# Kernel optimization log

Measured on AMD Instinct MI355X. Metric: run time of the kernel, lower is better.

## Reference

```python
import jax, jax.numpy as jnp
import numpy as np

B, S, D = 8, 2048, 512
DK, DV = 64, 64

def setup_inputs() -> dict:
    key = jax.random.key(0)
    ks = jax.random.split(key, 9)
    glorot = lambda k, shape: jax.random.uniform(k, shape, jnp.float32, -1.0, 1.0) * np.sqrt(6.0 / (shape[0] + shape[-1] if len(shape) > 1 else shape[0] + 1))
    return {
        "x_q": jax.random.normal(ks[0], (B, S, D), jnp.float32),
        "x_k": jax.random.normal(ks[1], (B, S, D), jnp.float32),
        "x_v": jax.random.normal(ks[2], (B, S, D), jnp.float32),
        "Wq": glorot(ks[3], (D, DK)), "bq": glorot(ks[4], (DK,)),
        "Wk": glorot(ks[5], (D, DK)), "bk": glorot(ks[6], (DK,)),
        "Wv": glorot(ks[7], (D, DV)), "bv": glorot(ks[8], (DV,)),
    }

def reference(x_q, x_k, x_v, Wq, bq, Wk, bk, Wv, bv):
    q = jnp.einsum("bsd,dk->bsk", x_q, Wq) + bq          # [B,S,DK]
    k = jnp.einsum("bsd,dk->bsk", x_k, Wk) + bk          # [B,S,DK]
    v = jnp.einsum("bsd,dv->bsv", x_v, Wv) + bv          # [B,S,DV]
    scale = 1.0 / np.sqrt(DK).astype(np.float32)
    scores = jnp.einsum("bqk,bsk->bqs", q, k) * scale     # [B,S,S]
    attn = jax.nn.softmax(scores, axis=-1)
    return jnp.einsum("bqs,bsv->bqv", attn, v)            # [B,S,DV]
```

## Files before the change

### kernel.cpp

```cpp
#include <hip/hip_runtime.h>
#include <stdint.h>

typedef __bf16 bf16;
typedef __bf16 bf16x8 __attribute__((ext_vector_type(8)));
typedef float f32x4 __attribute__((ext_vector_type(4)));

struct alignas(8) U16x4 { uint16_t v[4]; };

__device__ __forceinline__ f32x4 mfma16(bf16x8 a, bf16x8 b, f32x4 c) {
    return __builtin_amdgcn_mfma_f32_16x16x32_bf16(a, b, c, 0, 0, 0);
}

__device__ __forceinline__ void gload_lds16(const void* g, void* l) {
    __builtin_amdgcn_global_load_lds(
        (const __attribute__((address_space(1))) uint32_t*)g,
        (__attribute__((address_space(3))) uint32_t*)l, 16, 0, 0);
}

__device__ __forceinline__ uint16_t bf_bits(bf16 v) {
    return __builtin_bit_cast(uint16_t, v);
}

__device__ __forceinline__ float bf2f(uint16_t u) {
    uint32_t x = (uint32_t)u << 16;
    return __builtin_bit_cast(float, x);
}

#define QSCALE 0.18033688011112042f

__global__ __launch_bounds__(256, 2)
void proj_kernel(const float* __restrict__ xq, const float* __restrict__ xk,
                 const float* __restrict__ xv,
                 const float* __restrict__ Wq, const float* __restrict__ bq,
                 const float* __restrict__ Wk, const float* __restrict__ bk,
                 const float* __restrict__ Wv, const float* __restrict__ bv,
                 uint16_t* __restrict__ q_ws, uint16_t* __restrict__ k_ws,
                 uint16_t* __restrict__ vt_ws)
{
    const int p = blockIdx.y;
    const float* x    = (p == 0) ? xq : (p == 1) ? xk : xv;
    const float* W    = (p == 0) ? Wq : (p == 1) ? Wk : Wv;
    const float* bias = (p == 0) ? bq : (p == 1) ? bk : bv;

    const int m0 = blockIdx.x * 64;
    const int t  = threadIdx.x;
    const int l  = t & 63;
    const int w  = t >> 6;

    __shared__ __align__(16) uint16_t sW[32768];

    const int arow = m0 + w * 16 + (l & 15);
    const int kg   = (l >> 4) * 8;
    const float* xrow = x + (size_t)arow * 512 + kg;

    float4 av0[8], av1[8];
    #pragma unroll
    for (int s = 0; s < 8; s++) {
        av0[s] = *(const float4*)(xrow + s * 32);
        av1[s] = *(const float4*)(xrow + s * 32 + 4);
    }

    {
        const int f2 = (t >> 6) & 3;
        const int n  = (t & 15) + 16 * f2;
        const int kq = ((t >> 4) & 3) * 8;
        #pragma unroll 4
        for (int r = 0; r < 16; r++) {
            const int k0 = r * 32 + kq;
            bf16x8 v;
            #pragma unroll
            for (int j = 0; j < 8; j++)
                v[j] = (bf16)W[(size_t)(k0 + j) * 64 + n];
            *(bf16x8*)((char*)sW + (r * 256 + t) * 16) = v;
        }
    }

    __syncthreads();

    f32x4 acc[4];
    const f32x4 zero = {0.f, 0.f, 0.f, 0.f};
    #pragma unroll
    for (int f = 0; f < 4; f++) acc[f] = zero;

    #pragma unroll
    for (int kt = 0; kt < 16; kt++) {
        const int slot = kt & 7;
        bf16x8 a;
        a[0] = (bf16)av0[slot].x; a[1] = (bf16)av0[slot].y;
        a[2] = (bf16)av0[slot].z; a[3] = (bf16)av0[slot].w;
        a[4] = (bf16)av1[slot].x; a[5] = (bf16)av1[slot].y;
        a[6] = (bf16)av1[slot].z; a[7] = (bf16)av1[slot].w;
        if (kt < 8) {
            const int kb = (kt + 8) * 32;
            av0[slot] = *(const float4*)(xrow + kb);
            av1[slot] = *(const float4*)(xrow + kb + 4);
        }
        #pragma unroll
        for (int f = 0; f < 4; f++) {
            bf16x8 bfr = *(const bf16x8*)((const char*)sW + ((kt * 4 + f) * 64 + l) * 16);
            acc[f] = mfma16(a, bfr, acc[f]);
        }
    }

    float bv4[4];
    #pragma unroll
    for (int f = 0; f < 4; f++) bv4[f] = bias[16 * f + (l & 15)];

    if (p < 2) {
        uint16_t* outp = (p == 0) ? q_ws : k_ws;
        const float scale = (p == 0) ? QSCALE : 1.0f;
        #pragma unroll
        for (int f = 0; f < 4; f++)
            #pragma unroll
            for (int r = 0; r < 4; r++) {
                const int row = m0 + w * 16 + (l >> 4) * 4 + r;
                const int col = 16 * f + (l & 15);
                outp[(size_t)row * 64 + col] = bf_bits((bf16)((acc[f][r] + bv4[f]) * scale));
            }
    } else {
        #pragma unroll
        for (int f = 0; f < 4; f++) {
            const int row0 = m0 + w * 16 + (l >> 4) * 4;
            const int col  = 16 * f + (l & 15);
            const int bb = row0 >> 11;
            const int s0 = row0 & 2047;
            U16x4 pk;
            #pragma unroll
            for (int r = 0; r < 4; r++)
                pk.v[r] = bf_bits((bf16)(acc[f][r] + bv4[f]));
            *(U16x4*)(vt_ws + ((size_t)bb * 64 + col) * 2048 + s0) = pk;
        }
    }
}

template <int NCHUNK>
__global__ __launch_bounds__(512, 4)
void attn_kernel(const uint16_t* __restrict__ q_ws, const uint16_t* __restrict__ k_ws,
                 const uint16_t* __restrict__ vt_ws, float* __restrict__ out,
                 uint16_t* __restrict__ O_part, float* __restrict__ l_arr)
{
    constexpr int NT = 32 / NCHUNK;
    const int qt = blockIdx.x, b = blockIdx.y, c = blockIdx.z;
    const int t = threadIdx.x, l = t & 63, w = t >> 6;
    const int q = l & 15, g = l >> 4;
    const int q0 = qt * 128;

    __shared__ __align__(16) uint16_t sK[2][64 * 64];
    __shared__ __align__(16) uint16_t sV[2][64 * 64];
    __shared__ __align__(16) uint16_t sP[8][16 * 72];

    const uint16_t* qp = q_ws + ((size_t)(b * 2048 + q0)) * 64;
    const uint16_t* kp = k_ws + (size_t)b * 2048 * 64;
    const uint16_t* vp = vt_ws + (size_t)b * 64 * 2048;

    bf16x8 aq[2];
    #pragma unroll
    for (int ks = 0; ks < 2; ks++)
        aq[ks] = *(const bf16x8*)(qp + (size_t)(w * 16 + q) * 64 + g * 8 + ks * 32);

    const f32x4 zero = {0.f, 0.f, 0.f, 0.f};
    f32x4 acco[4];
    #pragma unroll
    for (int f = 0; f < 4; f++) acco[f] = zero;
    float l_st = 0.f;

    auto stage = [&](int tile, int buf) {
        const int kv0  = tile * 64;
        const int row  = t >> 3;
        const int slot = (t & 7) ^ (row & 7);
        gload_lds16(kp + (size_t)(kv0 + row) * 64 + slot * 8,
                    (char*)sK[buf] + t * 16);
        gload_lds16(vp + (size_t)row * 2048 + kv0 + slot * 8,
                    (char*)sV[buf] + t * 16);
    };

    stage(c * NT, 0);
    __syncthreads();

    for (int i = 0; i < NT; i++) {
        const int buf = i & 1;
        if (i < NT - 1) stage(c * NT + i + 1, buf ^ 1);

        f32x4 accs[4];
        #pragma unroll
        for (int f = 0; f < 4; f++) accs[f] = zero;
        #pragma unroll
        for (int ks = 0; ks < 2; ks++) {
            const int kb = g * 16 + ks * 64;
            #pragma unroll
            for (int f = 0; f < 4; f++) {
                const int srow = q + 16 * f;
                bf16x8 bk = *(const bf16x8*)((const char*)sK[buf] + srow * 128 + (kb ^ ((srow & 7) << 4)));
                accs[f] = mfma16(bk, aq[ks], accs[f]);
            }
        }

        float rs = 0.f;
        #pragma unroll
        for (int f = 0; f < 4; f++) {
            U16x4 pk;
            #pragma unroll
            for (int r = 0; r < 4; r++) {
                const float pv = exp2f(accs[f][r]);
                rs += pv;
                pk.v[r] = bf_bits((bf16)pv);
            }
            const int byte = q * 144 + ((32 * f + 8 * g) ^ ((q & 7) << 4));
            *(U16x4*)((char*)sP[w] + byte) = pk;
        }
        rs += __shfl_xor(rs, 16);
        rs += __shfl_xor(rs, 32);
        l_st += rs;

        asm volatile("s_waitcnt lgkmcnt(0)" ::: "memory");

        #pragma unroll
        for (int ks = 0; ks < 2; ks++) {
            bf16x8 ap = *(const bf16x8*)((const char*)sP[w] + q * 144 + ((ks * 64 + g * 16) ^ ((q & 7) << 4)));
            const int kb = g * 16 + ks * 64;
            #pragma unroll
            for (int f = 0; f < 4; f++) {
                const int vrow = q + 16 * f;
                bf16x8 bv2 = *(const bf16x8*)((const char*)sV[buf] + vrow * 128 + (kb ^ ((vrow & 7) << 4)));
                acco[f] = mfma16(ap, bv2, acco[f]);
            }
        }
        __syncthreads();
    }

    if constexpr (NCHUNK == 1) {
        #pragma unroll
        for (int r = 0; r < 4; r++) {
            const float lb = __shfl(l_st, (g * 4 + r) + (l & 48));
            #pragma unroll
            for (int f = 0; f < 4; f++) {
                const int qrow = q0 + w * 16 + g * 4 + r;
                const int col  = 16 * f + q;
                out[((size_t)(b * 2048 + qrow)) * 64 + col] = acco[f][r] / lb;
            }
        }
    } else {
        #pragma unroll
        for (int f = 0; f < 4; f++)
            #pragma unroll
            for (int r = 0; r < 4; r++) {
                const int qrow = q0 + w * 16 + g * 4 + r;
                const int col  = 16 * f + q;
                O_part[((size_t)c * 16384 + b * 2048 + qrow) * 64 + col] =
                    bf_bits((bf16)acco[f][r]);
            }
        if (l < 16) {
            const size_t idx = (size_t)c * 16384 + b * 2048 + q0 + w * 16 + l;
            l_arr[idx] = l_st;
        }
    }
}

__global__ __launch_bounds__(256, 8)
void combine_kernel(const uint16_t* __restrict__ O_part,
                    const float* __restrict__ l_arr, float* __restrict__ out)
{
    const int b = blockIdx.y;
    const int r0 = (blockIdx.x >> 2) * 64 + (blockIdx.x & 3) * 16;
    const int t = threadIdx.x;
    const int col = t & 63;
    const int rg = t >> 6;

    #pragma unroll
    for (int pass = 0; pass < 4; pass++) {
        const int qrow = r0 + pass * 4 + rg;
        const size_t ridx = (size_t)b * 2048 + qrow;
        float L = 0.f;
        #pragma unroll
        for (int c = 0; c < 4; c++) L += l_arr[(size_t)c * 16384 + ridx];
        float acc = 0.f;
        #pragma unroll
        for (int c = 0; c < 4; c++)
            acc += bf2f(O_part[((size_t)c * 16384 + ridx) * 64 + col]);
        out[ridx * 64 + col] = acc / L;
    }
}

extern "C" void kernel_launch(void* const* d_in, const int* in_sizes, int n_in,
                              void* d_out, int out_size, void* d_ws, size_t ws_size,
                              hipStream_t stream) {
    const float* xq = (const float*)d_in[0];
    const float* xk = (const float*)d_in[1];
    const float* xv = (const float*)d_in[2];
    const float* Wq = (const float*)d_in[3];
    const float* bq = (const float*)d_in[4];
    const float* Wk = (const float*)d_in[5];
    const float* bk = (const float*)d_in[6];
    const float* Wv = (const float*)d_in[7];
    const float* bv = (const float*)d_in[8];

    uint16_t* q_ws  = (uint16_t*)d_ws;
    uint16_t* k_ws  = q_ws + (size_t)16384 * 64;
    uint16_t* vt_ws = k_ws + (size_t)16384 * 64;
    uint16_t* O_part = vt_ws + (size_t)16384 * 64;
    float* l_arr  = (float*)(O_part + (size_t)4 * 16384 * 64);
    float* out = (float*)d_out;

    const size_t need = (size_t)3 * 16384 * 64 * 2
                      + (size_t)4 * 16384 * 64 * 2
                      + (size_t)4 * 16384 * 4;

    proj_kernel<<<dim3(256, 3), 256, 0, stream>>>(xq, xk, xv, Wq, bq, Wk, bk, Wv, bv,
                                                  q_ws, k_ws, vt_ws);
    if (ws_size >= need) {
        attn_kernel<4><<<dim3(16, 8, 4), 512, 0, stream>>>(q_ws, k_ws, vt_ws, out,
                                                           O_part, l_arr);
        combine_kernel<<<dim3(128, 8), 256, 0, stream>>>(O_part, l_arr, out);
    } else {
        attn_kernel<1><<<dim3(16, 8, 1), 512, 0, stream>>>(q_ws, k_ws, vt_ws, out,
                                                           nullptr, nullptr);
    }
}
```

Baseline: 55.48 us.

## Stage projection weights in chunks and shrink x prefetch to raise occupancy

The projection kernel now stages W into LDS in four 128-row groups using a 16KB buffer instead of 64KB. The staging is interleaved into the K loop with extra barriers, and launch bounds allow three blocks per CU. The x prefetch ring shrinks from 8 to 4 slots and uses inline-asm global loads with manual vmcnt waits to keep loads in flight. The aim is to cut LDS and register pressure so more waves overlap memory latency. In exchange it adds barriers, and the hand-written waitcnt counting is fragile.

```diff
diff --git a/kernel.cpp b/kernel.cpp
--- a/kernel.cpp
+++ b/kernel.cpp
@@ -17,6 +17,10 @@
         (__attribute__((address_space(3))) uint32_t*)l, 16, 0, 0);
 }
 
+__device__ __forceinline__ void gload_f4(f32x4& dst, const float* p) {
+    asm volatile("global_load_dwordx4 %0, %1, off" : "=v"(dst) : "v"(p) : "memory");
+}
+
 __device__ __forceinline__ uint16_t bf_bits(bf16 v) {
     return __builtin_bit_cast(uint16_t, v);
 }
@@ -28,7 +32,7 @@
 
 #define QSCALE 0.18033688011112042f
 
-__global__ __launch_bounds__(256, 2)
+__global__ __launch_bounds__(256, 3)
 void proj_kernel(const float* __restrict__ xq, const float* __restrict__ xk,
                  const float* __restrict__ xv,
                  const float* __restrict__ Wq, const float* __restrict__ bq,
@@ -47,34 +51,35 @@
     const int l  = t & 63;
     const int w  = t >> 6;
 
-    __shared__ __align__(16) uint16_t sW[32768];
+    __shared__ __align__(16) uint16_t sW[8192];
 
     const int arow = m0 + w * 16 + (l & 15);
     const int kg   = (l >> 4) * 8;
     const float* xrow = x + (size_t)arow * 512 + kg;
 
-    float4 av0[8], av1[8];
-    #pragma unroll
-    for (int s = 0; s < 8; s++) {
-        av0[s] = *(const float4*)(xrow + s * 32);
-        av1[s] = *(const float4*)(xrow + s * 32 + 4);
-    }
-
-    {
-        const int f2 = (t >> 6) & 3;
-        const int n  = (t & 15) + 16 * f2;
-        const int kq = ((t >> 4) & 3) * 8;
-        #pragma unroll 4
-        for (int r = 0; r < 16; r++) {
-            const int k0 = r * 32 + kq;
+    auto stageW = [&](int grp) {
+        const int f  = (t >> 6) & 3;
+        const int l2 = t & 63;
+        const int n  = (l2 & 15) + 16 * f;
+        #pragma unroll
+        for (int r = 0; r < 4; r++) {
+            const int k0 = grp * 128 + r * 32 + ((l2 >> 4) & 3) * 8;
             bf16x8 v;
             #pragma unroll
             for (int j = 0; j < 8; j++)
                 v[j] = (bf16)W[(size_t)(k0 + j) * 64 + n];
-            *(bf16x8*)((char*)sW + (r * 256 + t) * 16) = v;
-        }
-    }
-
+            *(bf16x8*)((char*)sW + ((r * 4 + f) * 64 + l2) * 16) = v;
+        }
+    };
+
+    f32x4 xs0[4], xs1[4];
+    #pragma unroll
+    for (int s = 0; s < 4; s++) {
+        gload_f4(xs0[s], xrow + s * 32);
+        gload_f4(xs1[s], xrow + s * 32 + 4);
+    }
+
+    stageW(0);
     __syncthreads();
 
     f32x4 acc[4];
@@ -84,21 +89,33 @@
 
     #pragma unroll
     for (int kt = 0; kt < 16; kt++) {
-        const int slot = kt & 7;
+        const int slot = kt & 3;
+        const int k4   = kt & 3;
+
+        asm volatile("s_waitcnt vmcnt(6)" ::: "memory");
+        __builtin_amdgcn_sched_barrier(0);
+
         bf16x8 a;
-        a[0] = (bf16)av0[slot].x; a[1] = (bf16)av0[slot].y;
-        a[2] = (bf16)av0[slot].z; a[3] = (bf16)av0[slot].w;
-        a[4] = (bf16)av1[slot].x; a[5] = (bf16)av1[slot].y;
-        a[6] = (bf16)av1[slot].z; a[7] = (bf16)av1[slot].w;
-        if (kt < 8) {
-            const int kb = (kt + 8) * 32;
-            av0[slot] = *(const float4*)(xrow + kb);
-            av1[slot] = *(const float4*)(xrow + kb + 4);
-        }
+        a[0] = (bf16)xs0[slot][0]; a[1] = (bf16)xs0[slot][1];
+        a[2] = (bf16)xs0[slot][2]; a[3] = (bf16)xs0[slot][3];
+        a[4] = (bf16)xs1[slot][0]; a[5] = (bf16)xs1[slot][1];
+        a[6] = (bf16)xs1[slot][2]; a[7] = (bf16)xs1[slot][3];
+
         #pragma unroll
         for (int f = 0; f < 4; f++) {
-            bf16x8 bfr = *(const bf16x8*)((const char*)sW + ((kt * 4 + f) * 64 + l) * 16);
+            bf16x8 bfr = *(const bf16x8*)((const char*)sW + ((k4 * 4 + f) * 64 + l) * 16);
             acc[f] = mfma16(a, bfr, acc[f]);
+        }
+
+        if (kt < 12) {
+            gload_f4(xs0[slot], xrow + (kt + 4) * 32);
+            gload_f4(xs1[slot], xrow + (kt + 4) * 32 + 4);
+        }
+
+        if (kt == 3 || kt == 7 || kt == 11) {
+            __syncthreads();
+            stageW((kt + 1) >> 2);
+            __syncthreads();
         }
     }
 
@@ -123,12 +140,12 @@
             const int row0 = m0 + w * 16 + (l >> 4) * 4;
             const int col  = 16 * f + (l & 15);
             const int bb = row0 >> 11;
-            const int s0 = row0 & 2047;
+            const int s0v = row0 & 2047;
             U16x4 pk;
             #pragma unroll
             for (int r = 0; r < 4; r++)
                 pk.v[r] = bf_bits((bf16)(acc[f][r] + bv4[f]));
-            *(U16x4*)(vt_ws + ((size_t)bb * 64 + col) * 2048 + s0) = pk;
+            *(U16x4*)(vt_ws + ((size_t)bb * 64 + col) * 2048 + s0v) = pk;
         }
     }
 }
```

After: 50.89 us. -8.3%, faster.
